# Optimization experiments

Measured on AMD Instinct MI355X. Metric: run time of the kernel, lower is better.

## Reference

```python
import jax, jax.numpy as jnp
import numpy as np

B, T, C = 8, 2048, 1024
DFF = 4 * C
EPS = 1e-5


def _ln(h, w, b):
    mu = jnp.mean(h, axis=-1, keepdims=True)
    var = jnp.mean((h - mu) ** 2, axis=-1, keepdims=True)
    return (h - mu) * jax.lax.rsqrt(var + EPS) * w + b


def setup_inputs() -> dict:
    key = jax.random.key(0)
    ks = jax.random.split(key, 8)
    s = lambda fan_in: 1.0 / np.sqrt(fan_in)
    return {
        "x": jax.random.normal(ks[0], (B, T, C), jnp.float32),
        "w_router": jax.random.normal(ks[1], (1, C), jnp.float32) * s(C),
        "ln1_w": jnp.ones((C,), jnp.float32),
        "ln1_b": jnp.zeros((C,), jnp.float32),
        "w_qkv": jax.random.normal(ks[2], (3 * C, C), jnp.float32) * s(C),
        "b_qkv": jnp.zeros((3 * C,), jnp.float32),
        "w_o": jax.random.normal(ks[3], (C, C), jnp.float32) * s(C),
        "b_o": jnp.zeros((C,), jnp.float32),
        "ln2_w": jnp.ones((C,), jnp.float32),
        "ln2_b": jnp.zeros((C,), jnp.float32),
        "w_fc": jax.random.normal(ks[4], (DFF, C), jnp.float32) * s(C),
        "b_fc": jnp.zeros((DFF,), jnp.float32),
        "w_proj": jax.random.normal(ks[5], (C, DFF), jnp.float32) * s(DFF),
        "b_proj": jnp.zeros((C,), jnp.float32),
        "top_k": 1024,
        "n_head": 16,
    }


def _gpt2_block(h, ln1_w, ln1_b, w_qkv, b_qkv, w_o, b_o, ln2_w, ln2_b,
                w_fc, b_fc, w_proj, b_proj, n_head):
    Bq, S, Cm = h.shape
    dh = Cm // n_head
    a = _ln(h, ln1_w, ln1_b)
    qkv = a @ w_qkv.T + b_qkv                         # [B,S,3C]
    q, k, v = jnp.split(qkv, 3, axis=-1)
    q = q.reshape(Bq, S, n_head, dh)
    k = k.reshape(Bq, S, n_head, dh)
    v = v.reshape(Bq, S, n_head, dh)
    scores = jnp.einsum("bqhd,bkhd->bhqk", q, k) / np.sqrt(dh)
    causal = jnp.tril(jnp.ones((S, S), bool))
    scores = jnp.where(causal, scores, jnp.finfo(scores.dtype).min)
    probs = jax.nn.softmax(scores, axis=-1)
    attn = jnp.einsum("bhqk,bkhd->bqhd", probs, v).reshape(Bq, S, Cm)
    h = h + attn @ w_o.T + b_o
    m = _ln(h, ln2_w, ln2_b)
    mlp = jax.nn.gelu(m @ w_fc.T + b_fc, approximate=False) @ w_proj.T + b_proj
    return h + mlp


def reference(x, w_router, ln1_w, ln1_b, w_qkv, b_qkv, w_o, b_o,
              ln2_w, ln2_b, w_fc, b_fc, w_proj, b_proj, top_k, n_head):
    # STEP 1: router logits + top-k tokens (sorted by position)
    logits = (x @ w_router.T)[..., 0]                  # [B,T]
    weights, idx = jax.lax.top_k(logits, top_k)        # [B,K]
    order = jnp.argsort(idx, axis=1)
    idx = jnp.take_along_axis(idx, order, axis=1)
    weights = jnp.take_along_axis(weights, order, axis=1)
    # STEP 2: gather reduced sequence and run the block
    tokens = jnp.take_along_axis(x, idx[..., None], axis=1)   # [B,K,C]
    processed = _gpt2_block(tokens, ln1_w, ln1_b, w_qkv, b_qkv, w_o, b_o,
                            ln2_w, ln2_b, w_fc, b_fc, w_proj, b_proj, n_head)
    # STEP 3: weighted scatter-add combine
    src = processed * weights[..., None]
    out = jax.vmap(lambda xb, ib, sb: xb.at[ib].add(sb))(x, idx, src)
    return out
```

## Files before the change

kernel.cpp:

```cpp
#include <hip/hip_runtime.h>
#include <hip/hip_bf16.h>

#define B_ 8
#define T_ 2048
#define C_ 1024
#define S_ 1024
#define H_ 16
#define DH_ 64
#define DFF_ 4096
#define M_ (B_*S_)

typedef __attribute__((ext_vector_type(8))) short bf16x8;
typedef __attribute__((ext_vector_type(4))) float f32x4;

__device__ __forceinline__ short f2bf(float f) {
  __hip_bfloat16 h = __float2bfloat16(f);
  return *reinterpret_cast<short*>(&h);
}
__device__ __forceinline__ float bf2f(short s) {
  __hip_bfloat16 h = *reinterpret_cast<__hip_bfloat16*>(&s);
  return __bfloat162float(h);
}

typedef const __attribute__((address_space(1))) unsigned int* gas_p;
typedef __attribute__((address_space(3))) unsigned int* las_p;
__device__ __forceinline__ void gload_lds16(const void* g, void* l) {
  __builtin_amdgcn_global_load_lds((gas_p)g, (las_p)l, 16, 0, 0);
}

__global__ __launch_bounds__(256) void k_router(const float* __restrict__ x,
    const float* __restrict__ wr, float* __restrict__ logits) {
  int tok = blockIdx.x * 4 + (threadIdx.x >> 6);
  int l = threadIdx.x & 63;
  const float* xr = x + (size_t)tok * C_;
  float s = 0.f;
  #pragma unroll
  for (int j = 0; j < C_/64; ++j) s += xr[l + 64*j] * wr[l + 64*j];
  #pragma unroll
  for (int m = 32; m; m >>= 1) s += __shfl_xor(s, m);
  if (l == 0) logits[tok] = s;
}

__global__ __launch_bounds__(1024) void k_topk(const float* __restrict__ logits,
    int* __restrict__ idx, float* __restrict__ wts) {
  __shared__ unsigned long long key[2048];
  int b = blockIdx.x, t = threadIdx.x;
  for (int i = t; i < T_; i += 1024) {
    float v = logits[(size_t)b*T_ + i];
    unsigned u = __float_as_uint(v);
    unsigned so = u ^ ((u >> 31) ? 0xFFFFFFFFu : 0x80000000u);
    key[i] = ((unsigned long long)(~so) << 32) | (unsigned)i;
  }
  __syncthreads();
  for (int k = 2; k <= 2048; k <<= 1) {
    for (int j = k >> 1; j > 0; j >>= 1) {
      int i = ((t & ~(j-1)) << 1) | (t & (j-1));
      int ix = i | j;
      unsigned long long a = key[i], c = key[ix];
      bool up = ((i & k) == 0);
      if ((a > c) == up) { key[i] = c; key[ix] = a; }
      __syncthreads();
    }
  }
  unsigned long long a = key[t];
  __syncthreads();
  unsigned i0 = (unsigned)(a & 0xFFFFFFFFu);
  unsigned so = ~(unsigned)(a >> 32);
  unsigned bits = (so & 0x80000000u) ? (so ^ 0x80000000u) : ~so;
  key[t] = ((unsigned long long)i0 << 32) | bits;
  __syncthreads();
  for (int k = 2; k <= 1024; k <<= 1) {
    for (int j = k >> 1; j > 0; j >>= 1) {
      if (t < 512) {
        int i = ((t & ~(j-1)) << 1) | (t & (j-1));
        int ix = i | j;
        unsigned long long a2 = key[i], c2 = key[ix];
        bool up = ((i & k) == 0);
        if ((a2 > c2) == up) { key[i] = c2; key[ix] = a2; }
      }
      __syncthreads();
    }
  }
  idx[(size_t)b*S_ + t] = (int)(key[t] >> 32);
  wts[(size_t)b*S_ + t] = __uint_as_float((unsigned)(key[t] & 0xFFFFFFFFu));
}

__global__ __launch_bounds__(256) void k_cvt(const float* __restrict__ s,
    short* __restrict__ d, int n4) {
  int i = blockIdx.x * 256 + threadIdx.x;
  if (i >= n4) return;
  float4 v = ((const float4*)s)[i];
  short4 o;
  o.x = f2bf(v.x); o.y = f2bf(v.y); o.z = f2bf(v.z); o.w = f2bf(v.w);
  ((short4*)d)[i] = o;
}

template<bool GATHER>
__global__ __launch_bounds__(256) void k_ln(const float* __restrict__ x,
    const int* __restrict__ idx, float* __restrict__ hbuf,
    short* __restrict__ obf, const float* __restrict__ g,
    const float* __restrict__ beta) {
  __shared__ float red[8];
  int row = blockIdx.x;
  const float* src;
  if (GATHER) {
    int b = row >> 10, k = row & 1023;
    src = x + ((size_t)b*T_ + idx[b*S_ + k]) * C_;
  } else {
    src = hbuf + (size_t)row * C_;
  }
  int t = threadIdx.x;
  float4 v = *(const float4*)(src + t*4);
  float s  = v.x + v.y + v.z + v.w;
  float s2 = v.x*v.x + v.y*v.y + v.z*v.z + v.w*v.w;
  #pragma unroll
  for (int m = 32; m; m >>= 1) { s += __shfl_xor(s, m); s2 += __shfl_xor(s2, m); }
  int w = t >> 6, lane = t & 63;
  if (lane == 0) { red[w] = s; red[w+4] = s2; }
  __syncthreads();
  s  = red[0]+red[1]+red[2]+red[3];
  s2 = red[4]+red[5]+red[6]+red[7];
  float mu = s * (1.f/(float)C_);
  float var = s2 * (1.f/(float)C_) - mu*mu;
  float rs = rsqrtf(var + 1e-5f);
  int c0 = t*4;
  float4 gw = *(const float4*)(g + c0);
  float4 bw = *(const float4*)(beta + c0);
  short4 o;
  o.x = f2bf((v.x-mu)*rs*gw.x + bw.x);
  o.y = f2bf((v.y-mu)*rs*gw.y + bw.y);
  o.z = f2bf((v.z-mu)*rs*gw.z + bw.z);
  o.w = f2bf((v.w-mu)*rs*gw.w + bw.w);
  *(short4*)(obf + (size_t)row*C_ + c0) = o;
  if (GATHER) *(float4*)(hbuf + (size_t)row*C_ + c0) = v;
}

#define EPI_BF16 0
#define EPI_GELU 1
#define EPI_ADD32 2

__device__ __forceinline__ float gelu_fast(float v) {
  float z = 0.7978845608f * (v + 0.044715f * v * v * v);
  float e = __expf(2.f * z);
  return v - v * __builtin_amdgcn_rcpf(e + 1.f);
}

template<int EPI>
__global__ __launch_bounds__(512, 2) void k_gemm5(
    const short* __restrict__ A, int lda,
    const short* __restrict__ Bp, int ldb,
    void* __restrict__ Cp, int ldc,
    const float* __restrict__ bias,
    int nNt, int Ktot) {
  constexpr int BM = 256, BN = 128;
  __shared__ short As[3][BM*64];
  __shared__ short Bs[3][BN*64];
  int nwg = gridDim.x, orig = blockIdx.x;
  int q8 = nwg >> 3, r8 = nwg & 7;
  int xcd = orig & 7, loc = orig >> 3;
  int wg = (xcd < r8 ? xcd*(q8+1) : r8*(q8+1) + (xcd-r8)*q8) + loc;
  int bm = wg / nNt, bn = wg % nNt;
  const short* Ar = A + (size_t)bm*BM*lda;
  const short* Br = Bp + (size_t)bn*BN*ldb;
  int t = threadIdx.x, lane = t & 63, w = t >> 6;
  int wm = w >> 1, wn = w & 1;
  int lr = lane & 15, kq = lane >> 4;

  auto stage = [&](int buf, int kt) {
    int k0 = kt << 6;
    #pragma unroll
    for (int c = 0; c < 4; ++c) {
      int ch = c*512 + t;
      int row = ch >> 3, sq = (ch & 7) ^ (row & 7);
      gload_lds16(Ar + (size_t)row*lda + (k0 + sq*8), &As[buf][ch*8]);
    }
    #pragma unroll
    for (int c = 0; c < 2; ++c) {
      int ch = c*512 + t;
      int row = ch >> 3, sq = (ch & 7) ^ (row & 7);
      gload_lds16(Br + (size_t)row*ldb + (k0 + sq*8), &Bs[buf][ch*8]);
    }
  };

  f32x4 acc[4][4] = {};
  int NT = Ktot >> 6;
  stage(0, 0);
  if (NT > 1) stage(1, 1);
  for (int kt = 0; kt < NT; ++kt) {
    int cur = kt % 3;
    if (kt + 1 < NT) asm volatile("s_waitcnt vmcnt(6)" ::: "memory");
    else             asm volatile("s_waitcnt vmcnt(0)" ::: "memory");
    __builtin_amdgcn_s_barrier();
    __builtin_amdgcn_sched_barrier(0);
    if (kt + 2 < NT) stage((kt + 2) % 3, kt + 2);
    bf16x8 af[2][4], bfv[2][4];
    #pragma unroll
    for (int ks = 0; ks < 2; ++ks) {
      #pragma unroll
      for (int i = 0; i < 4; ++i) {
        int ra = wm*64 + i*16 + lr;
        af[ks][i] = *(const bf16x8*)&As[cur][ra*64 + ((((ks<<2)+kq) ^ (ra & 7)) << 3)];
      }
      #pragma unroll
      for (int j = 0; j < 4; ++j) {
        int rb = wn*64 + j*16 + lr;
        bfv[ks][j] = *(const bf16x8*)&Bs[cur][rb*64 + ((((ks<<2)+kq) ^ (rb & 7)) << 3)];
      }
    }
    asm volatile("s_waitcnt lgkmcnt(0)" ::: "memory");
    __builtin_amdgcn_sched_barrier(0);
    #pragma unroll
    for (int ks = 0; ks < 2; ++ks)
      #pragma unroll
      for (int i = 0; i < 4; ++i)
        #pragma unroll
        for (int j = 0; j < 4; ++j)
          acc[i][j] = __builtin_amdgcn_mfma_f32_16x16x32_bf16(bfv[ks][j], af[ks][i], acc[i][j], 0, 0, 0);
  }
  int mrow0 = bm*BM + wm*64 + lr;
  int ncol0 = bn*BN + wn*64 + (kq << 2);
  #pragma unroll
  for (int i = 0; i < 4; ++i) {
    int row = mrow0 + i*16;
    #pragma unroll
    for (int j = 0; j < 4; ++j) {
      int col = ncol0 + j*16;
      float4 bv = bias ? *(const float4*)(bias + col) : make_float4(0.f,0.f,0.f,0.f);
      float v0 = acc[i][j][0] + bv.x, v1 = acc[i][j][1] + bv.y;
      float v2 = acc[i][j][2] + bv.z, v3 = acc[i][j][3] + bv.w;
      if (EPI == EPI_ADD32) {
        float* Co = (float*)Cp + (size_t)row*ldc + col;
        float4 old = *(float4*)Co;
        old.x += v0; old.y += v1; old.z += v2; old.w += v3;
        *(float4*)Co = old;
      } else {
        if (EPI == EPI_GELU) {
          v0 = gelu_fast(v0); v1 = gelu_fast(v1);
          v2 = gelu_fast(v2); v3 = gelu_fast(v3);
        }
        short4 o; o.x = f2bf(v0); o.y = f2bf(v1); o.z = f2bf(v2); o.w = f2bf(v3);
        *(short4*)((short*)Cp + (size_t)row*ldc + col) = o;
      }
    }
  }
}

__global__ __launch_bounds__(256) void k_vt(const short* __restrict__ qkv,
                                            short* __restrict__ vt) {
  __shared__ short tile[64][65];
  int blk = blockIdx.x;
  int s0 = (blk & 15) << 6;
  int bh = blk >> 4;
  int b = bh >> 4, h = bh & 15;
  const short* src = qkv + (size_t)b*S_*3*C_ + 2*C_ + h*DH_;
  int t = threadIdx.x;
  #pragma unroll
  for (int it = 0; it < 16; ++it) {
    int e = it*256 + t;
    int r = e >> 6, d = e & 63;
    tile[d][r] = src[(size_t)(s0 + r)*3*C_ + d];
  }
  __syncthreads();
  short* dst = vt + (size_t)bh*DH_*S_ + s0;
  #pragma unroll
  for (int it = 0; it < 16; ++it) {
    int e = it*256 + t;
    int d2 = e >> 6, c = e & 63;
    dst[(size_t)d2*S_ + c] = tile[d2][c];
  }
}

__global__ __launch_bounds__(256, 4) void k_fattn(
    const short* __restrict__ qkv, const short* __restrict__ vt,
    short* __restrict__ attnb) {
  __shared__ short Ks[2][64*64];
  __shared__ short Ps[4][32*72];
  int qt = blockIdx.x;
  int bh = blockIdx.y;
  int b = bh >> 4, h = bh & 15;
  int t = threadIdx.x, lane = t & 63, w = t >> 6;
  int lr = lane & 15, kq = lane >> 4;
  const short* Qbase = qkv + ((size_t)b*S_ + qt*128)*3*C_ + h*DH_;
  const short* Kbase = qkv + (size_t)b*S_*3*C_ + C_ + h*DH_;
  const short* Vtb   = vt + (size_t)bh*DH_*S_;

  short* Qs = &Ks[0][0];
  #pragma unroll
  for (int c = 0; c < 4; ++c) {
    int ch = c*256 + t;
    int row = ch >> 3, sq = (ch & 7) ^ (row & 7);
    gload_lds16(Qbase + (size_t)row*3*C_ + sq*8, &Qs[ch*8]);
  }
  asm volatile("s_waitcnt vmcnt(0)" ::: "memory");
  __builtin_amdgcn_s_barrier();
  bf16x8 qf[2][2];
  #pragma unroll
  for (int ks = 0; ks < 2; ++ks)
    #pragma unroll
    for (int i = 0; i < 2; ++i) {
      int rq = w*32 + i*16 + lr;
      qf[ks][i] = *(const bf16x8*)&Qs[rq*64 + ((((ks<<2)+kq) ^ (rq & 7)) << 3)];
    }
  asm volatile("s_waitcnt lgkmcnt(0)" ::: "memory");
  __builtin_amdgcn_sched_barrier(0);
  __builtin_amdgcn_s_barrier();

  auto stageK = [&](int buf, int jj) {
    #pragma unroll
    for (int c = 0; c < 2; ++c) {
      int ch = c*256 + t;
      int row = ch >> 3, sq = (ch & 7) ^ (row & 7);
      gload_lds16(Kbase + (size_t)(jj*64 + row)*3*C_ + sq*8, &Ks[buf][ch*8]);
    }
  };
  stageK(0, 0);

  f32x4 o[2][4] = {};
  float m_i[2] = {-3.0e38f, -3.0e38f};
  float l_i[2] = {0.f, 0.f};
  short* Pw = &Ps[w][0];
  int NTl = 2*qt + 2;

  for (int jj = 0; jj < NTl; ++jj) {
    int cur = jj & 1;
    asm volatile("s_waitcnt vmcnt(0)" ::: "memory");
    __builtin_amdgcn_s_barrier();
    if (jj + 1 < NTl) stageK(cur ^ 1, jj + 1);

    f32x4 s[2][4] = {};
    #pragma unroll
    for (int ks = 0; ks < 2; ++ks) {
      bf16x8 kf[4];
      #pragma unroll
      for (int j = 0; j < 4; ++j) {
        int rk = j*16 + lr;
        kf[j] = *(const bf16x8*)&Ks[cur][rk*64 + ((((ks<<2)+kq) ^ (rk & 7)) << 3)];
      }
      #pragma unroll
      for (int i = 0; i < 2; ++i)
        #pragma unroll
        for (int j = 0; j < 4; ++j)
          s[i][j] = __builtin_amdgcn_mfma_f32_16x16x32_bf16(kf[j], qf[ks][i], s[i][j], 0, 0, 0);
    }

    bool maskTile = (jj >= 2*qt);
    #pragma unroll
    for (int i = 0; i < 2; ++i) {
      int qrow = qt*128 + w*32 + i*16 + lr;
      float rmax = -3.0e38f;
      #pragma unroll
      for (int j = 0; j < 4; ++j)
        #pragma unroll
        for (int r = 0; r < 4; ++r) {
          int colg = jj*64 + j*16 + (kq<<2) + r;
          float v = s[i][j][r] * 0.125f;
          if (maskTile && colg > qrow) v = -3.0e38f;
          s[i][j][r] = v;
          rmax = fmaxf(rmax, v);
        }
      rmax = fmaxf(rmax, __shfl_xor(rmax, 16));
      rmax = fmaxf(rmax, __shfl_xor(rmax, 32));
      float mnew = fmaxf(m_i[i], rmax);
      float alpha = __expf(m_i[i] - mnew);
      m_i[i] = mnew;
      float rsum = 0.f;
      #pragma unroll
      for (int j = 0; j < 4; ++j)
        #pragma unroll
        for (int r = 0; r < 4; ++r) {
          float pv = __expf(s[i][j][r] - mnew);
          s[i][j][r] = pv;
          rsum += pv;
        }
      rsum += __shfl_xor(rsum, 16);
      rsum += __shfl_xor(rsum, 32);
      l_i[i] = l_i[i]*alpha + rsum;
      #pragma unroll
      for (int jo = 0; jo < 4; ++jo)
        #pragma unroll
        for (int r = 0; r < 4; ++r)
          o[i][jo][r] *= alpha;
    }

    #pragma unroll
    for (int i = 0; i < 2; ++i)
      #pragma unroll
      for (int j = 0; j < 4; ++j) {
        short4 pk;
        pk.x = f2bf(s[i][j][0]); pk.y = f2bf(s[i][j][1]);
        pk.z = f2bf(s[i][j][2]); pk.w = f2bf(s[i][j][3]);
        *(short4*)&Pw[(i*16 + lr)*72 + j*16 + (kq<<2)] = pk;
      }
    asm volatile("s_waitcnt lgkmcnt(0)" ::: "memory");
    __builtin_amdgcn_sched_barrier(0);

    #pragma unroll
    for (int sstep = 0; sstep < 2; ++sstep) {
      bf16x8 pf[2], vf[4];
      #pragma unroll
      for (int i = 0; i < 2; ++i)
        pf[i] = *(const bf16x8*)&Pw[(i*16 + lr)*72 + sstep*32 + (kq<<3)];
      #pragma unroll
      for (int jo = 0; jo < 4; ++jo)
        vf[jo] = *(const bf16x8*)&Vtb[(size_t)(jo*16 + lr)*S_ + jj*64 + sstep*32 + (kq<<3)];
      #pragma unroll
      for (int i = 0; i < 2; ++i)
        #pragma unroll
        for (int jo = 0; jo < 4; ++jo)
          o[i][jo] = __builtin_amdgcn_mfma_f32_16x16x32_bf16(vf[jo], pf[i], o[i][jo], 0, 0, 0);
    }
  }

  #pragma unroll
  for (int i = 0; i < 2; ++i) {
    float inv = 1.f / l_i[i];
    int q = qt*128 + w*32 + i*16 + lr;
    #pragma unroll
    for (int jo = 0; jo < 4; ++jo) {
      int d = jo*16 + (kq<<2);
      short4 ov;
      ov.x = f2bf(o[i][jo][0]*inv); ov.y = f2bf(o[i][jo][1]*inv);
      ov.z = f2bf(o[i][jo][2]*inv); ov.w = f2bf(o[i][jo][3]*inv);
      *(short4*)&attnb[((size_t)b*S_ + q)*C_ + h*DH_ + d] = ov;
    }
  }
}

__global__ void k_copy(const float* __restrict__ src, float* __restrict__ dst,
                       size_t n4) {
  size_t i = (size_t)blockIdx.x*256 + threadIdx.x;
  size_t stride = (size_t)gridDim.x*256;
  for (; i < n4; i += stride) ((float4*)dst)[i] = ((const float4*)src)[i];
}

__global__ __launch_bounds__(256) void k_scatter(const float* __restrict__ x,
    const int* __restrict__ idx, const float* __restrict__ wts,
    const float* __restrict__ hbuf, float* __restrict__ out) {
  int row = blockIdx.x;
  int b = row >> 10, k = row & 1023;
  int tk = idx[(size_t)b*S_ + k];
  float wv = wts[(size_t)b*S_ + k];
  size_t o  = ((size_t)b*T_ + tk)*C_ + threadIdx.x*4;
  size_t hs = (size_t)row*C_ + threadIdx.x*4;
  float4 xv = *(const float4*)(x + o);
  float4 hv = *(const float4*)(hbuf + hs);
  xv.x += wv*hv.x; xv.y += wv*hv.y; xv.z += wv*hv.z; xv.w += wv*hv.w;
  *(float4*)(out + o) = xv;
}

extern "C" void kernel_launch(void* const* d_in, const int* in_sizes, int n_in,
                              void* d_out, int out_size, void* d_ws, size_t ws_size,
                              hipStream_t stream) {
  const float* x     = (const float*)d_in[0];
  const float* wrt   = (const float*)d_in[1];
  const float* ln1w  = (const float*)d_in[2];
  const float* ln1b  = (const float*)d_in[3];
  const float* wqkv  = (const float*)d_in[4];
  const float* bqkv  = (const float*)d_in[5];
  const float* wo    = (const float*)d_in[6];
  const float* bo    = (const float*)d_in[7];
  const float* ln2w  = (const float*)d_in[8];
  const float* ln2b  = (const float*)d_in[9];
  const float* wfc   = (const float*)d_in[10];
  const float* bfc   = (const float*)d_in[11];
  const float* wproj = (const float*)d_in[12];
  const float* bproj = (const float*)d_in[13];
  float* out = (float*)d_out;

  char* p = (char*)d_ws;
  auto alloc = [&](size_t bytes) {
    char* r = p; p += (bytes + 255) & ~(size_t)255; return r;
  };
  float* logits = (float*)alloc((size_t)B_*T_*4);
  int*   idx    = (int*)  alloc((size_t)B_*S_*4);
  float* wts    = (float*)alloc((size_t)B_*S_*4);
  float* hbuf   = (float*)alloc((size_t)M_*C_*4);
  short* abuf   = (short*)alloc((size_t)M_*C_*2);
  short* qkvb   = (short*)alloc((size_t)M_*3*C_*2);
  short* vtb    = (short*)alloc((size_t)B_*H_*DH_*S_*2);
  short* attnb  = (short*)alloc((size_t)M_*C_*2);
  short* fcb    = (short*)alloc((size_t)M_*DFF_*2);
  short* wqkvb  = (short*)alloc((size_t)3*C_*C_*2);
  short* wob    = (short*)alloc((size_t)C_*C_*2);
  short* wfcb   = (short*)alloc((size_t)DFF_*C_*2);
  short* wprojb = (short*)alloc((size_t)C_*DFF_*2);
  if (ws_size < (size_t)(p - (char*)d_ws)) return;

  k_cvt<<<dim3(3*C_*C_/4/256), dim3(256), 0, stream>>>(wqkv, wqkvb, 3*C_*C_/4);
  k_cvt<<<dim3(C_*C_/4/256),   dim3(256), 0, stream>>>(wo, wob, C_*C_/4);
  k_cvt<<<dim3(DFF_*C_/4/256), dim3(256), 0, stream>>>(wfc, wfcb, DFF_*C_/4);
  k_cvt<<<dim3(C_*DFF_/4/256), dim3(256), 0, stream>>>(wproj, wprojb, C_*DFF_/4);

  k_router<<<dim3(B_*T_/4), dim3(256), 0, stream>>>(x, wrt, logits);
  k_topk<<<dim3(B_), dim3(1024), 0, stream>>>(logits, idx, wts);

  k_ln<true><<<dim3(M_), dim3(256), 0, stream>>>(x, idx, hbuf, abuf, ln1w, ln1b);

  k_gemm5<EPI_BF16><<<dim3((M_/256)*(3*C_/128)), dim3(512), 0, stream>>>(
      abuf, C_, wqkvb, C_, qkvb, 3*C_, bqkv, 3*C_/128, C_);

  k_vt<<<dim3(B_*H_*(S_/64)), dim3(256), 0, stream>>>(qkvb, vtb);

  k_fattn<<<dim3(S_/128, B_*H_), dim3(256), 0, stream>>>(qkvb, vtb, attnb);

  k_gemm5<EPI_ADD32><<<dim3((M_/256)*(C_/128)), dim3(512), 0, stream>>>(
      attnb, C_, wob, C_, hbuf, C_, bo, C_/128, C_);

  k_ln<false><<<dim3(M_), dim3(256), 0, stream>>>(nullptr, nullptr, hbuf, abuf, ln2w, ln2b);

  k_gemm5<EPI_GELU><<<dim3((M_/256)*(DFF_/128)), dim3(512), 0, stream>>>(
      abuf, C_, wfcb, C_, fcb, DFF_, bfc, DFF_/128, C_);

  k_gemm5<EPI_ADD32><<<dim3((M_/256)*(C_/128)), dim3(512), 0, stream>>>(
      fcb, DFF_, wprojb, DFF_, hbuf, C_, bproj, C_/128, DFF_);

  k_copy<<<dim3(2048), dim3(256), 0, stream>>>(x, out, (size_t)B_*T_*C_/4);
  k_scatter<<<dim3(M_), dim3(256), 0, stream>>>(x, idx, wts, hbuf, out);
}
```

Measured before the change: 547.9 us.

## Rework GEMM pipeline to double-buffered interleaved prefetch with templated 256-wide N tiles

```diff
diff --git a/kernel.cpp b/kernel.cpp
--- a/kernel.cpp
+++ b/kernel.cpp
@@ -145,16 +145,19 @@
   return v - v * __builtin_amdgcn_rcpf(e + 1.f);
 }
 
-template<int EPI>
-__global__ __launch_bounds__(512, 2) void k_gemm5(
+template<int BN, int EPI>
+__global__ __launch_bounds__(512, 2) void k_gemm6(
     const short* __restrict__ A, int lda,
     const short* __restrict__ Bp, int ldb,
     void* __restrict__ Cp, int ldc,
     const float* __restrict__ bias,
     int nNt, int Ktot) {
-  constexpr int BM = 256, BN = 128;
-  __shared__ short As[3][BM*64];
-  __shared__ short Bs[3][BN*64];
+  constexpr int BM = 256;
+  constexpr int WN_CNT = BN/64, WM_CNT = 8/WN_CNT;
+  constexpr int WM = BM/WM_CNT, FI = WM/16, PH = FI/2;
+  constexpr int BCH = BN/64;
+  __shared__ short As[2][BM*64];
+  __shared__ short Bs[2][BN*64];
   int nwg = gridDim.x, orig = blockIdx.x;
   int q8 = nwg >> 3, r8 = nwg & 7;
   int xcd = orig & 7, loc = orig >> 3;
@@ -163,64 +166,82 @@
   const short* Ar = A + (size_t)bm*BM*lda;
   const short* Br = Bp + (size_t)bn*BN*ldb;
   int t = threadIdx.x, lane = t & 63, w = t >> 6;
-  int wm = w >> 1, wn = w & 1;
+  int wm = w / WN_CNT, wn = w % WN_CNT;
   int lr = lane & 15, kq = lane >> 4;
 
-  auto stage = [&](int buf, int kt) {
-    int k0 = kt << 6;
-    #pragma unroll
-    for (int c = 0; c < 4; ++c) {
-      int ch = c*512 + t;
-      int row = ch >> 3, sq = (ch & 7) ^ (row & 7);
-      gload_lds16(Ar + (size_t)row*lda + (k0 + sq*8), &As[buf][ch*8]);
-    }
-    #pragma unroll
-    for (int c = 0; c < 2; ++c) {
-      int ch = c*512 + t;
-      int row = ch >> 3, sq = (ch & 7) ^ (row & 7);
-      gload_lds16(Br + (size_t)row*ldb + (k0 + sq*8), &Bs[buf][ch*8]);
-    }
+  auto stageA1 = [&](int buf, int kt, int c) {
+    int ch = c*512 + t;
+    int row = ch >> 3, sq = (ch & 7) ^ (row & 7);
+    gload_lds16(Ar + (size_t)row*lda + ((kt << 6) + sq*8), &As[buf][ch*8]);
   };
-
-  f32x4 acc[4][4] = {};
+  auto stageB1 = [&](int buf, int kt, int c) {
+    int ch = c*512 + t;
+    int row = ch >> 3, sq = (ch & 7) ^ (row & 7);
+    gload_lds16(Br + (size_t)row*ldb + ((kt << 6) + sq*8), &Bs[buf][ch*8]);
+  };
+
+  f32x4 acc[FI][4] = {};
   int NT = Ktot >> 6;
-  stage(0, 0);
-  if (NT > 1) stage(1, 1);
+  #pragma unroll
+  for (int c = 0; c < 4; ++c) stageA1(0, 0, c);
+  #pragma unroll
+  for (int c = 0; c < BCH; ++c) stageB1(0, 0, c);
+  asm volatile("s_waitcnt vmcnt(0)" ::: "memory");
+  __builtin_amdgcn_s_barrier();
+
   for (int kt = 0; kt < NT; ++kt) {
-    int cur = kt % 3;
-    if (kt + 1 < NT) asm volatile("s_waitcnt vmcnt(6)" ::: "memory");
-    else             asm volatile("s_waitcnt vmcnt(0)" ::: "memory");
-    __builtin_amdgcn_s_barrier();
-    __builtin_amdgcn_sched_barrier(0);
-    if (kt + 2 < NT) stage((kt + 2) % 3, kt + 2);
-    bf16x8 af[2][4], bfv[2][4];
+    int cur = kt & 1;
+    bool pre = (kt + 1 < NT);
+    const short* Ab = As[cur];
+    const short* Bb = Bs[cur];
     #pragma unroll
     for (int ks = 0; ks < 2; ++ks) {
-      #pragma unroll
-      for (int i = 0; i < 4; ++i) {
-        int ra = wm*64 + i*16 + lr;
-        af[ks][i] = *(const bf16x8*)&As[cur][ra*64 + ((((ks<<2)+kq) ^ (ra & 7)) << 3)];
+      bf16x8 bfv[4];
+      #pragma unroll
+      for (int ih = 0; ih < 2; ++ih) {
+        if (ks == 0 && pre) {
+          if (ih == 0) {
+            stageA1(cur ^ 1, kt + 1, 0); stageA1(cur ^ 1, kt + 1, 1);
+            stageB1(cur ^ 1, kt + 1, 0);
+            if (BCH > 1) stageB1(cur ^ 1, kt + 1, 1);
+          } else {
+            stageA1(cur ^ 1, kt + 1, 2); stageA1(cur ^ 1, kt + 1, 3);
+            if (BCH > 2) { stageB1(cur ^ 1, kt + 1, 2); stageB1(cur ^ 1, kt + 1, 3); }
+          }
+        }
+        if (ih == 0) {
+          #pragma unroll
+          for (int j = 0; j < 4; ++j) {
+            int rb = wn*64 + j*16 + lr;
+            bfv[j] = *(const bf16x8*)&Bb[rb*64 + ((((ks<<2)+kq) ^ (rb & 7)) << 3)];
+          }
+        }
+        bf16x8 af[PH];
+        #pragma unroll
+        for (int ii = 0; ii < PH; ++ii) {
+          int ra = wm*WM + (ih*PH + ii)*16 + lr;
+          af[ii] = *(const bf16x8*)&Ab[ra*64 + ((((ks<<2)+kq) ^ (ra & 7)) << 3)];
+        }
+        __builtin_amdgcn_s_setprio(1);
+        #pragma unroll
+        for (int ii = 0; ii < PH; ++ii)
+          #pragma unroll
+          for (int j = 0; j < 4; ++j)
+            acc[ih*PH + ii][j] = __builtin_amdgcn_mfma_f32_16x16x32_bf16(
+                bfv[j], af[ii], acc[ih*PH + ii][j], 0, 0, 0);
+        __builtin_amdgcn_s_setprio(0);
+        __builtin_amdgcn_sched_barrier(0);
       }
-      #pragma unroll
-      for (int j = 0; j < 4; ++j) {
-        int rb = wn*64 + j*16 + lr;
-        bfv[ks][j] = *(const bf16x8*)&Bs[cur][rb*64 + ((((ks<<2)+kq) ^ (rb & 7)) << 3)];
-      }
-    }
-    asm volatile("s_waitcnt lgkmcnt(0)" ::: "memory");
-    __builtin_amdgcn_sched_barrier(0);
-    #pragma unroll
-    for (int ks = 0; ks < 2; ++ks)
-      #pragma unroll
-      for (int i = 0; i < 4; ++i)
-        #pragma unroll
-        for (int j = 0; j < 4; ++j)
-          acc[i][j] = __builtin_amdgcn_mfma_f32_16x16x32_bf16(bfv[ks][j], af[ks][i], acc[i][j], 0, 0, 0);
-  }
-  int mrow0 = bm*BM + wm*64 + lr;
+    }
+    if (pre) {
+      asm volatile("s_waitcnt vmcnt(0)" ::: "memory");
+      __builtin_amdgcn_s_barrier();
+    }
+  }
+  int mrow0 = bm*BM + wm*WM + lr;
   int ncol0 = bn*BN + wn*64 + (kq << 2);
   #pragma unroll
-  for (int i = 0; i < 4; ++i) {
+  for (int i = 0; i < FI; ++i) {
     int row = mrow0 + i*16;
     #pragma unroll
     for (int j = 0; j < 4; ++j) {
@@ -496,22 +517,22 @@
 
   k_ln<true><<<dim3(M_), dim3(256), 0, stream>>>(x, idx, hbuf, abuf, ln1w, ln1b);
 
-  k_gemm5<EPI_BF16><<<dim3((M_/256)*(3*C_/128)), dim3(512), 0, stream>>>(
-      abuf, C_, wqkvb, C_, qkvb, 3*C_, bqkv, 3*C_/128, C_);
+  k_gemm6<256,EPI_BF16><<<dim3((M_/256)*(3*C_/256)), dim3(512), 0, stream>>>(
+      abuf, C_, wqkvb, C_, qkvb, 3*C_, bqkv, 3*C_/256, C_);
 
   k_vt<<<dim3(B_*H_*(S_/64)), dim3(256), 0, stream>>>(qkvb, vtb);
 
   k_fattn<<<dim3(S_/128, B_*H_), dim3(256), 0, stream>>>(qkvb, vtb, attnb);
 
-  k_gemm5<EPI_ADD32><<<dim3((M_/256)*(C_/128)), dim3(512), 0, stream>>>(
+  k_gemm6<128,EPI_ADD32><<<dim3((M_/256)*(C_/128)), dim3(512), 0, stream>>>(
       attnb, C_, wob, C_, hbuf, C_, bo, C_/128, C_);
 
   k_ln<false><<<dim3(M_), dim3(256), 0, stream>>>(nullptr, nullptr, hbuf, abuf, ln2w, ln2b);
 
-  k_gemm5<EPI_GELU><<<dim3((M_/256)*(DFF_/128)), dim3(512), 0, stream>>>(
-      abuf, C_, wfcb, C_, fcb, DFF_, bfc, DFF_/128, C_);
-
-  k_gemm5<EPI_ADD32><<<dim3((M_/256)*(C_/128)), dim3(512), 0, stream>>>(
+  k_gemm6<256,EPI_GELU><<<dim3((M_/256)*(DFF_/256)), dim3(512), 0, stream>>>(
+      abuf, C_, wfcb, C_, fcb, DFF_, bfc, DFF_/256, C_);
+
+  k_gemm6<128,EPI_ADD32><<<dim3((M_/256)*(C_/128)), dim3(512), 0, stream>>>(
       fcb, DFF_, wprojb, DFF_, hbuf, C_, bproj, C_/128, DFF_);
 
   k_copy<<<dim3(2048), dim3(256), 0, stream>>>(x, out, (size_t)B_*T_*C_/4);
```

Result: no change. 549.4 us (+0.3%).
